# Kernel optimization log

Hardware: AMD Instinct MI355X
Metric: run time of the kernel (lower is better)

The kernel has to match this reference:

```python
import jax, jax.numpy as jnp
import numpy as np

NUM_HEAD = 16
EMB_DIM = 1024
HEAD_DIM = EMB_DIM // NUM_HEAD

def setup_inputs() -> dict:
    key = jax.random.key(0)
    ks = jax.random.split(key, 9)
    B, S, D = 2, 2048, EMB_DIM
    s = 1.0 / np.sqrt(D)
    return {
        "x": jax.random.normal(ks[0], (B, S, D), dtype=jnp.float32),
        "Wq": jax.random.normal(ks[1], (D, D), dtype=jnp.float32) * s,
        "bq": jnp.zeros((D,), dtype=jnp.float32),
        "Wk": jax.random.normal(ks[2], (D, D), dtype=jnp.float32) * s,
        "bk": jnp.zeros((D,), dtype=jnp.float32),
        "Wv": jax.random.normal(ks[3], (D, D), dtype=jnp.float32) * s,
        "bv": jnp.zeros((D,), dtype=jnp.float32),
        "Wo": jax.random.normal(ks[4], (D, D), dtype=jnp.float32) * s,
        "bo": jnp.zeros((D,), dtype=jnp.float32),
    }

def reference(x, Wq, bq, Wk, bk, Wv, bv, Wo, bo):
    B, S, D = x.shape
    H, Hd = NUM_HEAD, HEAD_DIM
    # projections (torch Linear: x @ W.T + b; here W stored as [in, out])
    Q = (x @ Wq + bq).reshape(B, S, H, Hd)
    K = (x @ Wk + bk).reshape(B, S, H, Hd)
    V = (x @ Wv + bv).reshape(B, S, H, Hd)
    scale = jnp.sqrt(jnp.asarray(Hd, dtype=x.dtype))
    scores = jnp.einsum('bqhd,bkhd->bhqk', Q, K) / scale  # [B,H,S,S]
    attn = jax.nn.softmax(scores, axis=-1)
    out = jnp.einsum('bhql,blhd->bqhd', attn, V).reshape(B, S, D)
    return out @ Wo + bo
```

## Files before the change

kernel.cpp:

```cpp
#include <hip/hip_runtime.h>
#include <math.h>


using bf16   = __bf16;
using bf16x8 = __attribute__((ext_vector_type(8))) __bf16;
using bf16x4 = __attribute__((ext_vector_type(4))) __bf16;
using f32x4  = __attribute__((ext_vector_type(4))) float;

#define MFMA16(a, b, c) __builtin_amdgcn_mfma_f32_16x16x32_bf16((a), (b), (c), 0, 0, 0)
#define WAIT_VM0() asm volatile("s_waitcnt vmcnt(0)" ::: "memory")
#define WAITBAR(N) asm volatile("s_waitcnt vmcnt(" #N ")\n\ts_barrier" ::: "memory")

__device__ __forceinline__ bf16x8 ld8(const bf16* p) { return *(const bf16x8*)p; }

__device__ __forceinline__ void ldg_lds16(bf16* lds_base, const bf16* g) {
    __builtin_amdgcn_global_load_lds(
        (const __attribute__((address_space(1))) void*)g,
        (__attribute__((address_space(3))) void*)lds_base, 16, 0, 0);
}

__device__ __forceinline__ float fast_exp2(float x) {
#if __has_builtin(__builtin_amdgcn_exp2f)
    return __builtin_amdgcn_exp2f(x);
#else
    return exp2f(x);
#endif
}

__global__ __launch_bounds__(256) void prep_kernel(
    const float* __restrict__ x, const float* __restrict__ Wq,
    const float* __restrict__ Wk, const float* __restrict__ Wv,
    const float* __restrict__ Wo, bf16* __restrict__ xb,
    bf16* __restrict__ WtBase) {
    const int z = blockIdx.z;
    const int tid = threadIdx.x;
    if (z == 4) {
        int id = blockIdx.y * 32 + blockIdx.x;
#pragma unroll
        for (int k = 0; k < 4; ++k) {
            int i = id * 4096 + k * 1024 + tid * 4;
            float4 v = *(const float4*)&x[i];
            bf16x4 o = { (bf16)v.x, (bf16)v.y, (bf16)v.z, (bf16)v.w };
            *(bf16x4*)&xb[i] = o;
        }
        return;
    }
    __shared__ float tile[32][33];
    const float* W = (z == 0) ? Wq : (z == 1) ? Wk : (z == 2) ? Wv : Wo;
    bf16* Wt = WtBase + (size_t)z * 1024 * 1024;
    const int tx = tid & 31, ty = tid >> 5;
    const int x0 = blockIdx.x * 32, y0 = blockIdx.y * 32;
#pragma unroll
    for (int i = 0; i < 4; ++i)
        tile[ty + i * 8][tx] = W[(size_t)(y0 + ty + i * 8) * 1024 + x0 + tx];
    __syncthreads();
#pragma unroll
    for (int i = 0; i < 4; ++i)
        Wt[(size_t)(x0 + ty + i * 8) * 1024 + y0 + tx] = (bf16)tile[tx][ty + i * 8];
}

__device__ __forceinline__ void gemm_stage(const bf16* __restrict__ src, int r0,
                                           int k0, bf16* dst, int w, int lane) {
#pragma unroll
    for (int c = 0; c < 2; ++c) {
        int flat = (w * 2 + c) * 64 + lane;
        int row = flat >> 2, cc = flat & 3;
        int gk = (cc ^ ((row >> 1) & 3)) * 8;
        ldg_lds16(dst + (size_t)(w * 2 + c) * 512,
                  src + (size_t)(r0 + row) * 1024 + k0 + gk);
    }
}

__device__ __forceinline__ void gemm_core_128(const bf16* __restrict__ A,
                                              const bf16* __restrict__ Bt,
                                              int m0, int n0,
                                              bf16* As, bf16* Bs,
                                              f32x4 (&acc)[4][4]) {
    const int tid = threadIdx.x, lane = tid & 63, w = tid >> 6;
    const int lo = lane & 15, quad = lane >> 4;
    const int wm = w >> 1, wn = w & 1;

    gemm_stage(A,  m0, 0, As, w, lane);
    gemm_stage(Bt, n0, 0, Bs, w, lane);
    WAIT_VM0();
    __syncthreads();

    for (int it = 0; it < 32; ++it) {
        const int buf = it & 1;
        if (it + 1 < 32) {
            gemm_stage(A,  m0, (it + 1) * 32, As + (buf ^ 1) * 4096, w, lane);
            gemm_stage(Bt, n0, (it + 1) * 32, Bs + (buf ^ 1) * 4096, w, lane);
        }
        const bf16* Ab = As + buf * 4096;
        const bf16* Bb = Bs + buf * 4096;
        bf16x8 af[4], bq[4];
#pragma unroll
        for (int t = 0; t < 4; ++t) {
            int r = wm * 64 + t * 16 + lo;
            af[t] = ld8(&Ab[r * 32 + ((quad ^ ((r >> 1) & 3)) * 8)]);
        }
#pragma unroll
        for (int t = 0; t < 4; ++t) {
            int r = wn * 64 + t * 16 + lo;
            bq[t] = ld8(&Bb[r * 32 + ((quad ^ ((r >> 1) & 3)) * 8)]);
        }
#pragma unroll
        for (int mt = 0; mt < 4; ++mt)
#pragma unroll
            for (int nt = 0; nt < 4; ++nt)
                acc[mt][nt] = MFMA16(af[mt], bq[nt], acc[mt][nt]);
        WAIT_VM0();
        __syncthreads();
    }
}

__global__ __launch_bounds__(256, 3) void qkv_gemm_kernel(
    const bf16* __restrict__ Xb, const bf16* __restrict__ Wts,
    const float* __restrict__ bq, const float* __restrict__ bk,
    const float* __restrict__ bv,
    bf16* __restrict__ Qo, bf16* __restrict__ Ko, bf16* __restrict__ Vto) {
    __shared__ bf16 Smem[4 * 4096];
    bf16* As = Smem;
    bf16* Bs = Smem + 2 * 4096;
    const int z = blockIdx.z;
    const bf16*  Bt   = Wts + (size_t)z * 1024 * 1024;
    const float* bias = (z == 0) ? bq : (z == 1) ? bk : bv;
    const int m0 = blockIdx.y * 128, n0 = blockIdx.x * 128;

    f32x4 acc[4][4] = {};
    gemm_core_128(Xb, Bt, m0, n0, As, Bs, acc);

    const int tid = threadIdx.x;
    const int lane = tid & 63, w = tid >> 6;
    const int lo = lane & 15, quad = lane >> 4;
    const int wm = w >> 1, wn = w & 1;
    const float QSCALE = 0.125f * 1.44269504088896f;

    if (z == 2) {
        bf16* T = Smem;
        const int b = m0 >> 11;
        const int s_base = m0 & 2047;
#pragma unroll
        for (int half = 0; half < 2; ++half) {
            __syncthreads();
            if (wm == half) {
#pragma unroll
                for (int nt = 0; nt < 4; ++nt)
#pragma unroll
                    for (int mt = 0; mt < 4; ++mt)
#pragma unroll
                        for (int r = 0; r < 4; ++r) {
                            int nn = wn * 64 + nt * 16 + lo;
                            int mm = mt * 16 + quad * 4 + r;
                            T[nn * 68 + mm] = (bf16)(acc[mt][nt][r] + bias[n0 + nn]);
                        }
            }
            __syncthreads();
#pragma unroll
            for (int p = 0; p < 8; ++p) {
                int pos = p * 1024 + tid * 4;
                int row = pos >> 6, col = pos & 63;
                int n = n0 + row, h = n >> 6, hd = n & 63;
                int colp = (col & 32) | (((col >> 2) & 3) << 3)
                         | (((col >> 4) & 1) << 2) | (col & 3);
                bf16x4 v = *(const bf16x4*)&T[row * 68 + col];
                *(bf16x4*)&Vto[((size_t)((b * 16 + h) * 64 + hd) << 11)
                               + s_base + half * 64 + colp] = v;
            }
        }
    } else {
#pragma unroll
        for (int mt = 0; mt < 4; ++mt)
#pragma unroll
            for (int nt = 0; nt < 4; ++nt)
#pragma unroll
                for (int r = 0; r < 4; ++r) {
                    int m = m0 + wm * 64 + mt * 16 + quad * 4 + r;
                    int n = n0 + wn * 64 + nt * 16 + lo;
                    float v = acc[mt][nt][r] + bias[n];
                    int b = m >> 11, s = m & 2047, h = n >> 6, hd = n & 63;
                    if (z == 0)
                        Qo[((size_t)((b * 16 + h) * 2048 + s) << 6) + hd] = (bf16)(v * QSCALE);
                    else
                        Ko[((size_t)((b * 16 + h) * 2048 + s) << 6) + hd] = (bf16)v;
                }
    }
}

__global__ __launch_bounds__(256, 2) void out_gemm_kernel(
    const bf16* __restrict__ A, const bf16* __restrict__ Bt,
    const float* __restrict__ bo, float* __restrict__ Co) {
    __shared__ bf16 As[2 * 2048];
    __shared__ bf16 Bs[2 * 4096];
    const int tid = threadIdx.x, lane = tid & 63, w = tid >> 6;
    const int lo = lane & 15, quad = lane >> 4;
    const int wm = w >> 1, wn = w & 1;
    const int m0 = blockIdx.y * 64, n0 = blockIdx.x * 128;

    auto stageA = [&](int k0, bf16* dst) {
        int flat = w * 64 + lane;
        int row = flat >> 2, cc = flat & 3;
        int gk = (cc ^ ((row >> 1) & 3)) * 8;
        ldg_lds16(dst + (size_t)w * 512, A + (size_t)(m0 + row) * 1024 + k0 + gk);
    };
    auto stageB = [&](int k0, bf16* dst) {
#pragma unroll
        for (int c = 0; c < 2; ++c) {
            int flat = (w * 2 + c) * 64 + lane;
            int row = flat >> 2, cc = flat & 3;
            int gk = (cc ^ ((row >> 1) & 3)) * 8;
            ldg_lds16(dst + (size_t)(w * 2 + c) * 512,
                      Bt + (size_t)(n0 + row) * 1024 + k0 + gk);
        }
    };

    f32x4 acc[2][4] = {};
    stageA(0, As);
    stageB(0, Bs);
    WAIT_VM0();
    __syncthreads();

    for (int it = 0; it < 32; ++it) {
        const int buf = it & 1;
        if (it + 1 < 32) {
            stageA((it + 1) * 32, As + (buf ^ 1) * 2048);
            stageB((it + 1) * 32, Bs + (buf ^ 1) * 4096);
        }
        const bf16* Ab = As + buf * 2048;
        const bf16* Bb = Bs + buf * 4096;
        bf16x8 af[2], bq[4];
#pragma unroll
        for (int t = 0; t < 2; ++t) {
            int r = wm * 32 + t * 16 + lo;
            af[t] = ld8(&Ab[r * 32 + ((quad ^ ((r >> 1) & 3)) * 8)]);
        }
#pragma unroll
        for (int t = 0; t < 4; ++t) {
            int r = wn * 64 + t * 16 + lo;
            bq[t] = ld8(&Bb[r * 32 + ((quad ^ ((r >> 1) & 3)) * 8)]);
        }
#pragma unroll
        for (int mt = 0; mt < 2; ++mt)
#pragma unroll
            for (int nt = 0; nt < 4; ++nt)
                acc[mt][nt] = MFMA16(af[mt], bq[nt], acc[mt][nt]);
        WAIT_VM0();
        __syncthreads();
    }

#pragma unroll
    for (int mt = 0; mt < 2; ++mt)
#pragma unroll
        for (int nt = 0; nt < 4; ++nt)
#pragma unroll
            for (int r = 0; r < 4; ++r) {
                int m = m0 + wm * 32 + mt * 16 + quad * 4 + r;
                int n = n0 + wn * 64 + nt * 16 + lo;
                Co[(size_t)m * 1024 + n] = acc[mt][nt][r] + bo[n];
            }
}

__global__ __launch_bounds__(256, 2) void attn_kernel(
    const bf16* __restrict__ Q, const bf16* __restrict__ K,
    const bf16* __restrict__ Vt, bf16* __restrict__ AO) {
    __shared__ bf16 Ks[4][64 * 64];
    __shared__ bf16 Vs[4][64 * 64];
    const int tid = threadIdx.x, w = tid >> 6, lane = tid & 63;
    const int lo = lane & 15, quad = lane >> 4;
    const int blk = blockIdx.x;
    const int bh = (blk & 7) | ((blk >> 7) << 3);
    const int qb = (blk >> 3) & 15;
    const int q0 = qb * 128 + w * 32;

    const bf16* Qb = Q + ((size_t)bh * 2048 + q0) * 64;
    const bf16* Kb = K + (size_t)bh * 2048 * 64;
    const bf16* Vb = Vt + (size_t)bh * 64 * 2048;

    bf16x8 qa[2][2];
#pragma unroll
    for (int qt = 0; qt < 2; ++qt)
#pragma unroll
        for (int ks = 0; ks < 2; ++ks)
            qa[qt][ks] = ld8(&Qb[(qt * 16 + lo) * 64 + ks * 32 + quad * 8]);

    f32x4 O[2][4] = {};
    float l_acc[2] = { 0.f, 0.f };

    auto stage = [&](int s0, int buf) {
#pragma unroll
        for (int c = 0; c < 2; ++c) {
            int flat = (w * 2 + c) * 64 + lane;
            int row = flat >> 3, cc = flat & 7;
            int g = (cc ^ (row & 7)) * 8;
            ldg_lds16(&Ks[buf][(w * 2 + c) * 512], &Kb[(size_t)(s0 + row) * 64 + g]);
            ldg_lds16(&Vs[buf][(w * 2 + c) * 512], &Vb[(size_t)row * 2048 + s0 + g]);
        }
    };

    const int swz = lo & 7;

    auto qk = [&](int nb, f32x4 (&S)[2][4]) {
        const bf16* Kt = &Ks[nb][0];
#pragma unroll
        for (int qt = 0; qt < 2; ++qt)
#pragma unroll
            for (int t = 0; t < 4; ++t)
                S[qt][t] = f32x4{ 0.f, 0.f, 0.f, 0.f };
#pragma unroll
        for (int t = 0; t < 4; ++t) {
            int r = t * 16 + lo;
#pragma unroll
            for (int ks = 0; ks < 2; ++ks) {
                bf16x8 kf = ld8(&Kt[r * 64 + (((quad + 4 * ks) ^ swz) * 8)]);
                S[0][t] = MFMA16(kf, qa[0][ks], S[0][t]);
                S[1][t] = MFMA16(kf, qa[1][ks], S[1][t]);
            }
        }
    };

    auto expP = [&](f32x4 (&Sin)[2][4], bf16x8 (&pa)[2][2]) {
#pragma unroll
        for (int qt = 0; qt < 2; ++qt)
#pragma unroll
            for (int kc = 0; kc < 2; ++kc) {
                float e0 = fast_exp2(Sin[qt][2 * kc][0]);
                float e1 = fast_exp2(Sin[qt][2 * kc][1]);
                float e2 = fast_exp2(Sin[qt][2 * kc][2]);
                float e3 = fast_exp2(Sin[qt][2 * kc][3]);
                float e4 = fast_exp2(Sin[qt][2 * kc + 1][0]);
                float e5 = fast_exp2(Sin[qt][2 * kc + 1][1]);
                float e6 = fast_exp2(Sin[qt][2 * kc + 1][2]);
                float e7 = fast_exp2(Sin[qt][2 * kc + 1][3]);
                l_acc[qt] += ((e0 + e1) + (e2 + e3)) + ((e4 + e5) + (e6 + e7));
                pa[qt][kc] = bf16x8{ (bf16)e0, (bf16)e1, (bf16)e2, (bf16)e3,
                                     (bf16)e4, (bf16)e5, (bf16)e6, (bf16)e7 };
            }
    };

    auto pv = [&](int cb, bf16x8 (&pa)[2][2]) {
        const bf16* Vl = &Vs[cb][0];
#pragma unroll
        for (int kc = 0; kc < 2; ++kc)
#pragma unroll
            for (int nt = 0; nt < 4; ++nt) {
                int r = nt * 16 + lo;
                bf16x8 vf = ld8(&Vl[r * 64 + ((((kc * 4 + quad) ^ swz)) * 8)]);
                O[0][nt] = MFMA16(pa[0][kc], vf, O[0][nt]);
                O[1][nt] = MFMA16(pa[1][kc], vf, O[1][nt]);
            }
    };

    auto step = [&](f32x4 (&Sin)[2][4], f32x4 (&Sout)[2][4], int cb, int nb) {
        bf16x8 pa[2][2];
        expP(Sin, pa);
        qk(nb, Sout);
        pv(cb, pa);
    };

    stage(0, 0);
    stage(64, 1);
    WAITBAR(4);

    f32x4 Sa[2][4], Sb[2][4];
    qk(0, Sa);

    for (int it = 0; it < 30; it += 2) {
        stage((it + 2) * 64, (it + 2) & 3);
        WAITBAR(4);
        step(Sa, Sb, it & 3, (it + 1) & 3);
        stage((it + 3) * 64, (it + 3) & 3);
        WAITBAR(4);
        step(Sb, Sa, (it + 1) & 3, (it + 2) & 3);
    }
    WAITBAR(0);
    step(Sa, Sb, 2, 3);
    {
        bf16x8 pa[2][2];
        expP(Sb, pa);
        pv(3, pa);
    }

    const int bb = bh >> 4, h = bh & 15;
#pragma unroll
    for (int qt = 0; qt < 2; ++qt) {
        float lt = l_acc[qt];
        lt += __shfl_xor(lt, 16, 64);
        lt += __shfl_xor(lt, 32, 64);
        const size_t outbase = ((size_t)(bb * 2048 + q0 + qt * 16)) * 1024 + h * 64;
#pragma unroll
        for (int r = 0; r < 4; ++r) {
            float rl = 1.0f / __shfl(lt, quad * 4 + r, 64);
            size_t rowoff = outbase + (size_t)(quad * 4 + r) * 1024;
#pragma unroll
            for (int nt = 0; nt < 4; ++nt)
                AO[rowoff + nt * 16 + lo] = (bf16)(O[qt][nt][r] * rl);
        }
    }
}

extern "C" void kernel_launch(void* const* d_in, const int* in_sizes, int n_in,
                              void* d_out, int out_size, void* d_ws, size_t ws_size,
                              hipStream_t stream) {
    const float* x  = (const float*)d_in[0];
    const float* Wq = (const float*)d_in[1];
    const float* bq = (const float*)d_in[2];
    const float* Wk = (const float*)d_in[3];
    const float* bk = (const float*)d_in[4];
    const float* Wv = (const float*)d_in[5];
    const float* bv = (const float*)d_in[6];
    const float* Wo = (const float*)d_in[7];
    const float* bo = (const float*)d_in[8];
    float* out = (float*)d_out;

    bf16* wsb = (bf16*)d_ws;
    const size_t M1 = 1024u * 1024u;
    bf16* Xb  = wsb;
    bf16* AO  = wsb;
    bf16* Wt  = wsb + 4 * M1;
    bf16* Qw  = wsb + 8 * M1;
    bf16* Kw  = wsb + 12 * M1;
    bf16* Vtw = wsb + 16 * M1;

    prep_kernel<<<dim3(32, 32, 5), 256, 0, stream>>>(x, Wq, Wk, Wv, Wo, Xb, Wt);
    qkv_gemm_kernel<<<dim3(8, 32, 3), 256, 0, stream>>>(Xb, Wt, bq, bk, bv, Qw, Kw, Vtw);
    attn_kernel<<<512, 256, 0, stream>>>(Qw, Kw, Vtw, AO);
    out_gemm_kernel<<<dim3(8, 64), 256, 0, stream>>>(AO, Wt + 3 * M1, bo, out);
}
```

Baseline: 180.3 us.

## Load V fragments directly from global into registers instead of LDS staging

V tiles are no longer staged through shared memory. Each lane now loads its MFMA B-operand fragments straight from global memory into double-buffered registers one iteration ahead, and the vmcnt waits are retuned to the new load counts. This halves LDS usage and removes the LDS reads for V, at the cost of more VGPRs and uncoalesced 16-byte global loads that are each read by several waves without shared reuse.

New measurement: 205.6 us. 14.1% more time.

```diff
diff --git a/kernel.cpp b/kernel.cpp
--- a/kernel.cpp
+++ b/kernel.cpp
@@ -264,7 +264,6 @@
     const bf16* __restrict__ Q, const bf16* __restrict__ K,
     const bf16* __restrict__ Vt, bf16* __restrict__ AO) {
     __shared__ bf16 Ks[4][64 * 64];
-    __shared__ bf16 Vs[4][64 * 64];
     const int tid = threadIdx.x, w = tid >> 6, lane = tid & 63;
     const int lo = lane & 15, quad = lane >> 4;
     const int blk = blockIdx.x;
@@ -275,6 +274,7 @@
     const bf16* Qb = Q + ((size_t)bh * 2048 + q0) * 64;
     const bf16* Kb = K + (size_t)bh * 2048 * 64;
     const bf16* Vb = Vt + (size_t)bh * 64 * 2048;
+    const bf16* Vl = Vb + (size_t)lo * 2048 + quad * 8;
 
     bf16x8 qa[2][2];
 #pragma unroll
@@ -286,15 +286,22 @@
     f32x4 O[2][4] = {};
     float l_acc[2] = { 0.f, 0.f };
 
-    auto stage = [&](int s0, int buf) {
+    auto stageK = [&](int s0, int buf) {
 #pragma unroll
         for (int c = 0; c < 2; ++c) {
             int flat = (w * 2 + c) * 64 + lane;
             int row = flat >> 3, cc = flat & 7;
             int g = (cc ^ (row & 7)) * 8;
             ldg_lds16(&Ks[buf][(w * 2 + c) * 512], &Kb[(size_t)(s0 + row) * 64 + g]);
-            ldg_lds16(&Vs[buf][(w * 2 + c) * 512], &Vb[(size_t)row * 2048 + s0 + g]);
-        }
+        }
+    };
+
+    auto vload = [&](int s0, bf16x8 (&Vr)[2][4]) {
+#pragma unroll
+        for (int kc = 0; kc < 2; ++kc)
+#pragma unroll
+            for (int nt = 0; nt < 4; ++nt)
+                Vr[kc][nt] = ld8(Vl + (size_t)nt * 16 * 2048 + s0 + kc * 32);
     };
 
     const int swz = lo & 7;
@@ -337,47 +344,51 @@
             }
     };
 
-    auto pv = [&](int cb, bf16x8 (&pa)[2][2]) {
-        const bf16* Vl = &Vs[cb][0];
+    auto pv = [&](bf16x8 (&Vr)[2][4], bf16x8 (&pa)[2][2]) {
 #pragma unroll
         for (int kc = 0; kc < 2; ++kc)
 #pragma unroll
             for (int nt = 0; nt < 4; ++nt) {
-                int r = nt * 16 + lo;
-                bf16x8 vf = ld8(&Vl[r * 64 + ((((kc * 4 + quad) ^ swz)) * 8)]);
-                O[0][nt] = MFMA16(pa[0][kc], vf, O[0][nt]);
-                O[1][nt] = MFMA16(pa[1][kc], vf, O[1][nt]);
-            }
-    };
-
-    auto step = [&](f32x4 (&Sin)[2][4], f32x4 (&Sout)[2][4], int cb, int nb) {
+                O[0][nt] = MFMA16(pa[0][kc], Vr[kc][nt], O[0][nt]);
+                O[1][nt] = MFMA16(pa[1][kc], Vr[kc][nt], O[1][nt]);
+            }
+    };
+
+    auto step = [&](f32x4 (&Sin)[2][4], f32x4 (&Sout)[2][4], int nb,
+                    bf16x8 (&Vr)[2][4]) {
         bf16x8 pa[2][2];
         expP(Sin, pa);
         qk(nb, Sout);
-        pv(cb, pa);
-    };
-
-    stage(0, 0);
-    stage(64, 1);
-    WAITBAR(4);
+        pv(Vr, pa);
+    };
+
+    bf16x8 VA[2][4], VB[2][4];
+    vload(0, VB);
+    stageK(0, 0);
+    stageK(64, 1);
+    WAITBAR(0);
 
     f32x4 Sa[2][4], Sb[2][4];
     qk(0, Sa);
 
     for (int it = 0; it < 30; it += 2) {
-        stage((it + 2) * 64, (it + 2) & 3);
-        WAITBAR(4);
-        step(Sa, Sb, it & 3, (it + 1) & 3);
-        stage((it + 3) * 64, (it + 3) & 3);
-        WAITBAR(4);
-        step(Sb, Sa, (it + 1) & 3, (it + 2) & 3);
-    }
-    WAITBAR(0);
-    step(Sa, Sb, 2, 3);
+        vload((it + 1) * 64, VA);
+        stageK((it + 2) * 64, (it + 2) & 3);
+        WAITBAR(10);
+        step(Sa, Sb, (it + 1) & 3, VB);
+        vload((it + 2) * 64, VB);
+        stageK((it + 3) * 64, (it + 3) & 3);
+        WAITBAR(10);
+        step(Sb, Sa, (it + 2) & 3, VA);
+    }
+    vload(31 * 64, VA);
+    WAITBAR(8);
+    step(Sa, Sb, 3, VB);
+    WAIT_VM0();
     {
         bf16x8 pa[2][2];
         expP(Sb, pa);
-        pv(3, pa);
+        pv(VA, pa);
     }
 
     const int bb = bh >> 4, h = bh & 15;
```
